# Performance work log

Measured on AMD Instinct MI355X. Metric: run time of the kernel, lower is better.

Reference implementation:

```python
import jax, jax.numpy as jnp
import numpy as np

V, E, U, T, B = 32000, 256, 512, 32, 64

def setup_inputs() -> dict:
    key = jax.random.key(0)
    ks = jax.random.split(key, 12)
    return {
        "input_seq": jax.random.randint(ks[0], (B, T), 1, V),
        "target": jax.random.randint(ks[1], (B, T), 1, V),
        "encoder_output": jax.random.normal(ks[2], (B, T, U), jnp.float32),
        "enc_h": jax.random.normal(ks[3], (B, U), jnp.float32),
        "enc_c": jax.random.normal(ks[4], (B, U), jnp.float32),
        "emb": jax.random.normal(ks[5], (V, E), jnp.float32) * 0.02,
        "Wk": jax.random.normal(ks[6], (E, 4 * U), jnp.float32) * 0.05,
        "Wr": jax.random.normal(ks[7], (U, 4 * U), jnp.float32) * 0.05,
        "b": jnp.zeros((4 * U,), jnp.float32),
        "Wgen": jax.random.normal(ks[8], (2 * U + E, U), jnp.float32) * 0.05,
        "bgen": jnp.zeros((U,), jnp.float32),
    }


def _lstm(x, h0, c0, Wk, Wr, b):
    # x: [B,T,E]; Keras gate order i,f,c,o; returns seq of h [B,T,U], hT, cT
    xg = jnp.einsum('bte,eg->btg', x, Wk) + b  # precompute input projections
    def cell(carry, xg_t):
        h, c = carry
        g = xg_t + h @ Wr
        i, f, cc, o = jnp.split(g, 4, axis=-1)
        c_new = jax.nn.sigmoid(f) * c + jax.nn.sigmoid(i) * jnp.tanh(cc)
        h_new = jax.nn.sigmoid(o) * jnp.tanh(c_new)
        return (h_new, c_new), h_new
    (hT, cT), hs = jax.lax.scan(cell, (h0, c0), jnp.swapaxes(xg, 0, 1))
    return jnp.swapaxes(hs, 0, 1), hT, cT


def reference(input_seq, target, encoder_output, enc_h, enc_c, emb, Wk, Wr, b, Wgen, bgen):
    dec_in0 = emb[target]  # [B,T,E]
    def outer(carry, _):
        dec_in, h, c = carry
        outs, hT, cT = _lstm(dec_in, h, c, Wk, Wr, b)  # [B,T,U]
        h_b = jnp.broadcast_to(h[:, None, :], (B, T, U))  # pre-update state, per original
        feat = jnp.concatenate([encoder_output, h_b, dec_in], axis=-1)
        p_gen = jax.nn.sigmoid(feat @ Wgen + bgen)  # [B,T,U]
        idx = jnp.argmax(outs, axis=-1)  # greedy 'token' ids (as in original)
        new_in = emb[idx]
        return (new_in, hT, cT), (outs, p_gen, h, c)
    _, (dec_outs, p_gens, hs, cs) = jax.lax.scan(
        outer, (dec_in0, enc_h, enc_c), None, length=T - 1)
    return dec_outs, p_gens, hs, cs
```

## Files before the change

### kernel.cpp

```cpp
#include <hip/hip_runtime.h>
#include <math.h>

#define Bz 64
#define Tz 32
#define Uz 512
#define NITER 31
#define G4 2048

typedef unsigned long long ull;

__device__ __forceinline__ float sigf(float x) { return 1.f / (1.f + expf(-x)); }

#define AT_LOADF(p)   __hip_atomic_load((p), __ATOMIC_RELAXED, __HIP_MEMORY_SCOPE_AGENT)
#define AT_LOADI(p)   __hip_atomic_load((p), __ATOMIC_RELAXED, __HIP_MEMORY_SCOPE_AGENT)
#define AT_LOAD64(p)  __hip_atomic_load((p), __ATOMIC_RELAXED, __HIP_MEMORY_SCOPE_AGENT)
#define AT_STORE(p,v) __hip_atomic_store((p), (v), __ATOMIC_RELAXED, __HIP_MEMORY_SCOPE_AGENT)

__device__ __forceinline__ void poll32(const unsigned* fl, unsigned target) {
  const unsigned* f = &fl[(threadIdx.x & 31) * 16];
  unsigned v;
  do {
    v = __hip_atomic_load(f, __ATOMIC_RELAXED, __HIP_MEMORY_SCOPE_AGENT);
  } while (__any((int)(v < target)));
}

__global__ __launch_bounds__(256) void gemm_f32(
    const float* __restrict__ A, const int* __restrict__ Arows, int lda,
    const float* __restrict__ Bm, int ldb, const float* __restrict__ bias,
    float* __restrict__ C, int N, int K)
{
  __shared__ __align__(16) float As[16][68];
  __shared__ __align__(16) float Bs[16][68];
  const int tid = threadIdx.x;
  const int bm = blockIdx.y, bn = blockIdx.x;
  const int tx = tid & 15, ty = tid >> 4;
  float acc[4][4] = {{0.f}};
  const int sm = tid >> 2, sk = (tid & 3) * 4;
  const int arow = Arows ? Arows[bm * 64 + sm] : (bm * 64 + sm);
  const float* Ap = A + (size_t)arow * lda + sk;
  const int bk = tid >> 4, bn4 = (tid & 15) * 4;
  const float* Bp = Bm + (size_t)bk * ldb + bn * 64 + bn4;
  for (int kk = 0; kk < K; kk += 16) {
    float4 av = *(const float4*)(Ap + kk);
    float4 bv = *(const float4*)(Bp + (size_t)kk * ldb);
    As[sk + 0][sm] = av.x; As[sk + 1][sm] = av.y;
    As[sk + 2][sm] = av.z; As[sk + 3][sm] = av.w;
    *(float4*)&Bs[bk][bn4] = bv;
    __syncthreads();
#pragma unroll
    for (int kt = 0; kt < 16; ++kt) {
      float4 a = *(const float4*)&As[kt][ty * 4];
      float4 b = *(const float4*)&Bs[kt][tx * 4];
      acc[0][0] += a.x * b.x; acc[0][1] += a.x * b.y; acc[0][2] += a.x * b.z; acc[0][3] += a.x * b.w;
      acc[1][0] += a.y * b.x; acc[1][1] += a.y * b.y; acc[1][2] += a.y * b.z; acc[1][3] += a.y * b.w;
      acc[2][0] += a.z * b.x; acc[2][1] += a.z * b.y; acc[2][2] += a.z * b.z; acc[2][3] += a.z * b.w;
      acc[3][0] += a.w * b.x; acc[3][1] += a.w * b.y; acc[3][2] += a.w * b.z; acc[3][3] += a.w * b.w;
    }
    __syncthreads();
  }
  const int cm = bm * 64 + ty * 4, cn = bn * 64 + tx * 4;
  float bc0 = bias ? bias[cn + 0] : 0.f;
  float bc1 = bias ? bias[cn + 1] : 0.f;
  float bc2 = bias ? bias[cn + 2] : 0.f;
  float bc3 = bias ? bias[cn + 3] : 0.f;
#pragma unroll
  for (int i = 0; i < 4; ++i) {
    float4 o;
    o.x = acc[i][0] + bc0; o.y = acc[i][1] + bc1;
    o.z = acc[i][2] + bc2; o.w = acc[i][3] + bc3;
    *(float4*)&C[(size_t)(cm + i) * N + cn] = o;
  }
}

__global__ void init_kernel(unsigned* __restrict__ flags) {
  int i = blockIdx.x * blockDim.x + threadIdx.x;
  if (i < 8192) flags[i] = 0u;
}

#define DO_GEMM(HRED, GIDX, GV)                                                          \
  {                                                                                      \
    float4 a0 = {0,0,0,0}, a1 = {0,0,0,0}, a2 = {0,0,0,0}, a3 = {0,0,0,0};               \
    _Pragma("unroll")                                                                    \
    for (int kk = 0; kk < 16; ++kk) {                                                    \
      float4 hv = *(const float4*)&HRED[(kk * 32 + ks) * 4];                             \
      a0.x += hv.x * w4[kk].x; a0.y += hv.x * w4[kk].y;                                  \
      a0.z += hv.x * w4[kk].z; a0.w += hv.x * w4[kk].w;                                  \
      a1.x += hv.y * w4[kk].x; a1.y += hv.y * w4[kk].y;                                  \
      a1.z += hv.y * w4[kk].z; a1.w += hv.y * w4[kk].w;                                  \
      a2.x += hv.z * w4[kk].x; a2.y += hv.z * w4[kk].y;                                  \
      a2.z += hv.z * w4[kk].z; a2.w += hv.z * w4[kk].w;                                  \
      a3.x += hv.w * w4[kk].x; a3.y += hv.w * w4[kk].y;                                  \
      a3.z += hv.w * w4[kk].z; a3.w += hv.w * w4[kk].w;                                  \
    }                                                                                    \
    bool c1 = ks & 1, c2 = ks & 2, c3 = ks & 4, c4 = ks & 8;                             \
    float4 k0 = c1 ? a2 : a0, k1 = c1 ? a3 : a1;                                         \
    float4 s0 = c1 ? a0 : a2, s1 = c1 ? a1 : a3;                                         \
    k0.x += __shfl_xor(s0.x, 2); k0.y += __shfl_xor(s0.y, 2);                            \
    k0.z += __shfl_xor(s0.z, 2); k0.w += __shfl_xor(s0.w, 2);                            \
    k1.x += __shfl_xor(s1.x, 2); k1.y += __shfl_xor(s1.y, 2);                            \
    k1.z += __shfl_xor(s1.z, 2); k1.w += __shfl_xor(s1.w, 2);                            \
    float4 m0 = c2 ? k1 : k0, n0 = c2 ? k0 : k1;                                         \
    m0.x += __shfl_xor(n0.x, 4); m0.y += __shfl_xor(n0.y, 4);                            \
    m0.z += __shfl_xor(n0.z, 4); m0.w += __shfl_xor(n0.w, 4);                            \
    float q0 = c3 ? m0.z : m0.x, q1 = c3 ? m0.w : m0.y;                                  \
    float r0 = c3 ? m0.x : m0.z, r1 = c3 ? m0.y : m0.w;                                  \
    q0 += __shfl_xor(r0, 8); q1 += __shfl_xor(r1, 8);                                    \
    float u_ = c4 ? q1 : q0, v_ = c4 ? q0 : q1;                                          \
    u_ += __shfl_xor(v_, 16);                                                            \
    u_ += __shfl_xor(u_, 32);                                                            \
    if (lane < 32) g_l[GIDX][b_f][j_f] = u_ + (GV);                                      \
  }

__global__ __launch_bounds__(512, 1) void decoder_persist(
    const float* __restrict__ Wr,
    const float* __restrict__ Wgen,
    const float* __restrict__ bgen,
    const float* __restrict__ enc_h,
    const float* __restrict__ enc_c,
    const float* __restrict__ embW,
    const float* __restrict__ xg0,
    const float* __restrict__ enc_part,
    const float* __restrict__ dec0,
    const float* __restrict__ decW,
    float* __restrict__ hbT,
    int*   __restrict__ idxbuf,
    unsigned* __restrict__ flags,
    float* __restrict__ out)
{
  __shared__ __align__(16) float hredA[2048];
  __shared__ __align__(16) float hredB[2048];
  __shared__ __align__(16) float Wgenl[8192];
  __shared__ float g_l[2][4][68];
  __shared__ float hW_l[128];
  __shared__ float redl[512];
  __shared__ int   idx_l[8][32];
  __shared__ float bgen_l[16];

  const int tid = threadIdx.x;
  const int bid = blockIdx.x;
  const int pr = bid >> 5, ug = bid & 31;
  const int bA0 = pr * 4, bB0 = 32 + pr * 4;
  const int u0 = ug * 16;
  const int w = tid >> 6, lane = tid & 63;
  const int ks = lane >> 1, jsub = lane & 1;
  const int jloc = w * 8 + jsub * 4;
  const int gcol0 = (jloc >> 4) * Uz + u0 + (jloc & 15);
  const int b_f = 2 * (ks & 1) + ((ks >> 1) & 1);
  const int ji_f = 2 * ((ks >> 2) & 1) + ((ks >> 3) & 1);
  const int j_f = jloc + ji_f;
  const int gcol_f = (j_f >> 4) * Uz + u0 + (j_f & 15);
  const int p_b = lane >> 4, p_ul = lane & 15;

  float* out_dec = out;
  float* out_pg  = out + (size_t)NITER * Bz * Tz * Uz;
  float* out_hs  = out + 2 * (size_t)NITER * Bz * Tz * Uz;
  float* out_cs  = out_hs + (size_t)NITER * Bz * Uz;

  unsigned* flA = flags + (pr * 2 + 0) * 512;
  unsigned* flB = flags + (pr * 2 + 1) * 512;
  float* hbTp = hbT + pr * 8192;

  float4 w4[16];
#pragma unroll
  for (int kk = 0; kk < 16; ++kk)
    w4[kk] = *(const float4*)&Wr[(size_t)(kk * 32 + ks) * G4 + gcol0];
  for (int q = 0; q < 16; ++q) {
    int e = q * 512 + tid, k = e >> 4, ul = e & 15;
    Wgenl[k * 16 + ul] = Wgen[(size_t)(512 + k) * Uz + u0 + ul];
  }
  if (tid < 16) bgen_l[tid] = bgen[u0 + tid];
  {
    int k = tid;
#pragma unroll
    for (int b = 0; b < 4; ++b) {
      hredA[k * 4 + b] = enc_h[(size_t)(bA0 + b) * Uz + k];
      hredB[k * 4 + b] = enc_h[(size_t)(bB0 + b) * Uz + k];
    }
  }
  float c_reg = 0.f;
  if (w == 0) c_reg = enc_c[(size_t)(bA0 + p_b) * Uz + u0 + p_ul];
  if (w == 1) c_reg = enc_c[(size_t)(bB0 + p_b) * Uz + u0 + p_ul];
  __syncthreads();

#pragma unroll 1
  for (int s = 0; s < NITER; ++s) {
    const int* idxp = idxbuf + ((s + 1) & 1) * 2048;
    int*       idxq = idxbuf + (s & 1) * 2048;
    const unsigned base = 33u * s;

    if (s > 0) {
      if (w == 1 && lane < 32) poll32(flA, base);
      __syncthreads();
      if (tid < 128) {
        int pb = tid >> 4, t2 = (tid & 15) * 2;
        int batch = (pb < 4) ? bA0 + pb : bB0 + (pb - 4);
        idx_l[pb][t2]     = AT_LOADI(&idxp[batch * Tz + t2]);
        idx_l[pb][t2 + 1] = AT_LOADI(&idxp[batch * Tz + t2 + 1]);
      } else if (w >= 2 && w < 6) {
        int st = tid - 128;
        const ull* src = (const ull*)&hbTp[1 * 2048];
        ull* dst = (ull*)hredB;
#pragma unroll
        for (int q = 0; q < 4; ++q) dst[q * 256 + st] = AT_LOAD64(&src[q * 256 + st]);
      }
      __syncthreads();
    }
    {
      int g = tid >> 8, r6 = tid & 255, kq = r6 >> 6, l6 = r6 & 63;
      int b = l6 >> 4, ul = l6 & 15;
      const float* hr = g ? hredB : hredA;
      float a = 0.f;
#pragma unroll 8
      for (int k = kq * 128; k < kq * 128 + 128; ++k)
        a += hr[k * 4 + b] * Wgenl[k * 16 + ul];
      redl[tid] = a;
    }
    __syncthreads();
    if (tid < 128) {
      int g = tid >> 6, l6 = tid & 63;
      hW_l[tid] = (redl[g * 256 + l6] + redl[g * 256 + 64 + l6]) +
                  (redl[g * 256 + 128 + l6] + redl[g * 256 + 192 + l6]);
    }
    if (w < 2) {
      int batch = (w == 0 ? bA0 : bB0) + p_b;
      const float* hr = w ? hredB : hredA;
      out_hs[((size_t)s * Bz + batch) * Uz + u0 + p_ul] = hr[(u0 + p_ul) * 4 + p_b];
      out_cs[((size_t)s * Bz + batch) * Uz + u0 + p_ul] = c_reg;
    }
    __syncthreads();
#pragma unroll 1
    for (int i = 0; i < 8; ++i) {
      int o = i * 512 + tid;
      int ul = o & 15, t = (o >> 4) & 31, pb = o >> 9;
      int batch = (pb < 4) ? bA0 + pb : bB0 + (pb - 4);
      size_t r = (size_t)batch * Tz + t;
      float dv = (s == 0) ? dec0[r * Uz + u0 + ul]
                          : decW[(size_t)idx_l[pb][t] * Uz + u0 + ul];
      float v = enc_part[r * Uz + u0 + ul] + hW_l[(pb >> 2) * 64 + (pb & 3) * 16 + ul]
              + dv + bgen_l[ul];
      out_pg[(((size_t)s * Bz + batch) * Tz + t) * Uz + u0 + ul] = sigf(v);
    }

#pragma unroll 1
    for (int t = 0; t < Tz; ++t) {
      const int gt = s * Tz + t;
      ull stg[16];
      float gvA = 0.f, gvB = 0.f;
      if (lane < 32) {
        int rA = (bA0 + b_f) * Tz + t, rB = (bB0 + b_f) * Tz + t;
        if (s == 0) {
          gvA = xg0[(size_t)rA * G4 + gcol_f];
          gvB = xg0[(size_t)rB * G4 + gcol_f];
        } else {
          gvA = embW[(size_t)idx_l[b_f][t] * G4 + gcol_f];
          gvB = embW[(size_t)idx_l[4 + b_f][t] * G4 + gcol_f];
        }
      }
      if (w == 1 && gt > 0) {
        if (lane < 32) poll32(flB, base + t);
        const ull* src = (const ull*)&hbTp[((gt & 1) * 2 + 1) * 2048];
#pragma unroll
        for (int q = 0; q < 16; ++q) stg[q] = AT_LOAD64(&src[q * 64 + lane]);
      }
      DO_GEMM(hredA, 0, gvA);
      __syncthreads();
      if (w == 0) {
        float gi = g_l[0][p_b][p_ul],      gf = g_l[0][p_b][16 + p_ul];
        float gc = g_l[0][p_b][32 + p_ul], go = g_l[0][p_b][48 + p_ul];
        c_reg = sigf(gf) * c_reg + sigf(gi) * tanhf(gc);
        float hn = sigf(go) * tanhf(c_reg);
        int parw = (gt + 1) & 1;
        AT_STORE(&hbTp[(parw * 2 + 0) * 2048 + (u0 + p_ul) * 4 + p_b], hn);
        AT_STORE(&out_dec[(((size_t)s * Bz + bA0 + p_b) * Tz + t) * Uz + u0 + p_ul], hn);
        asm volatile("s_waitcnt vmcnt(0)" ::: "memory");
        if (lane == 0) AT_STORE(&flA[ug * 16], base + t + 1);
      } else if (w == 1 && gt > 0) {
        ull* dst = (ull*)hredB;
#pragma unroll
        for (int q = 0; q < 16; ++q) dst[q * 64 + lane] = stg[q];
      }
      __syncthreads();
      if (w == 6) {
        if (lane < 32) poll32(flA, base + t + 1);
        const ull* src = (const ull*)&hbTp[(((gt + 1) & 1) * 2 + 0) * 2048];
#pragma unroll
        for (int q = 0; q < 16; ++q) stg[q] = AT_LOAD64(&src[q * 64 + lane]);
      }
      DO_GEMM(hredB, 1, gvB);
      __syncthreads();
      if (w == 1) {
        float gi = g_l[1][p_b][p_ul],      gf = g_l[1][p_b][16 + p_ul];
        float gc = g_l[1][p_b][32 + p_ul], go = g_l[1][p_b][48 + p_ul];
        c_reg = sigf(gf) * c_reg + sigf(gi) * tanhf(gc);
        float hn = sigf(go) * tanhf(c_reg);
        int parw = (gt + 1) & 1;
        AT_STORE(&hbTp[(parw * 2 + 1) * 2048 + (u0 + p_ul) * 4 + p_b], hn);
        AT_STORE(&out_dec[(((size_t)s * Bz + bB0 + p_b) * Tz + t) * Uz + u0 + p_ul], hn);
        asm volatile("s_waitcnt vmcnt(0)" ::: "memory");
        if (lane == 0) AT_STORE(&flB[ug * 16], base + t + 1);
      } else if (w == 6) {
        ull* dst = (ull*)hredA;
#pragma unroll
        for (int q = 0; q < 16; ++q) dst[q * 64 + lane] = stg[q];
      }
      __syncthreads();
    }

    if (s < NITER - 1) {
      if (w == 1 && lane < 32) poll32(flB, base + 32);
      __syncthreads();
      {
        int R = ug * 8 + w;
        int pb = R >> 5, t = R & 31;
        int batch = (pb < 4) ? bA0 + pb : bB0 + (pb - 4);
        const float* row = &out_dec[(((size_t)s * Bz + batch) * Tz + t) * Uz];
        float bv = -3.4e38f; int bi = 0;
#pragma unroll
        for (int q = 0; q < 8; ++q) {
          int u = lane + q * 64;
          float v = AT_LOADF(&row[u]);
          if (v > bv) { bv = v; bi = u; }
        }
#pragma unroll
        for (int off = 1; off < 64; off <<= 1) {
          float ov = __shfl_xor(bv, off);
          int   oi = __shfl_xor(bi, off);
          if (ov > bv || (ov == bv && oi < bi)) { bv = ov; bi = oi; }
        }
        if (lane == 0) AT_STORE(&idxq[batch * Tz + t], bi);
      }
      asm volatile("s_waitcnt vmcnt(0)" ::: "memory");
      __syncthreads();
      if (tid == 0) {
        AT_STORE(&flA[ug * 16], base + 33);
        AT_STORE(&flB[ug * 16], base + 33);
      }
    }
  }
}

extern "C" void kernel_launch(void* const* d_in, const int* in_sizes, int n_in,
                              void* d_out, int out_size, void* d_ws, size_t ws_size,
                              hipStream_t stream) {
  const int*   target = (const int*)d_in[1];
  const float* enc    = (const float*)d_in[2];
  const float* enc_h  = (const float*)d_in[3];
  const float* enc_cp = (const float*)d_in[4];
  const float* emb    = (const float*)d_in[5];
  const float* Wk     = (const float*)d_in[6];
  const float* Wr     = (const float*)d_in[7];
  const float* bb     = (const float*)d_in[8];
  const float* Wgen   = (const float*)d_in[9];
  const float* bgen   = (const float*)d_in[10];
  float* out = (float*)d_out;

  float* ws = (float*)d_ws;
  float* hbT      = ws;
  float* embW     = ws + 65536;
  float* xg0      = ws + 1114112;
  float* enc_part = ws + 5308416;
  float* dec0     = ws + 6356992;
  float* decW     = ws + 7405568;
  int*   idxbuf   = (int*)(ws + 7667712);
  unsigned* flags = (unsigned*)(ws + 7671808);

  init_kernel<<<16, 512, 0, stream>>>(flags);
  gemm_f32<<<dim3(32, 8), 256, 0, stream>>>(emb, nullptr, 256, Wk, 2048, bb, embW, 2048, 256);
  gemm_f32<<<dim3(32, 32), 256, 0, stream>>>(emb, target, 256, Wk, 2048, bb, xg0, 2048, 256);
  gemm_f32<<<dim3(8, 32), 256, 0, stream>>>(enc, nullptr, 512, Wgen, 512, nullptr, enc_part, 512, 512);
  gemm_f32<<<dim3(8, 32), 256, 0, stream>>>(emb, target, 256, Wgen + 1024 * 512, 512, nullptr, dec0, 512, 256);
  gemm_f32<<<dim3(8, 8), 256, 0, stream>>>(emb, nullptr, 256, Wgen + 1024 * 512, 512, nullptr, decW, 512, 256);

  decoder_persist<<<256, 512, 0, stream>>>(Wr, Wgen, bgen, enc_h, enc_cp, embW, xg0,
      enc_part, dec0, decW, hbT, idxbuf, flags, out);
}
```

Measured before the change: 5.819 ms.

## Replace flag polling with sequence-tagged mailboxes and compute argmax locally per block

Hidden-state exchange between blocks now packs each h value with its global step tag into a 64-bit mailbox word. Consumers spin directly on the data, with loads issued before the GEMM and retried after it, so the separate flag store, vmcnt wait and flag poll are gone. The per-outer-iteration global argmax phase and its extra barrier are replaced by each block computing argmax from its replicated LDS copy of h as the steps go. This also removes the flag-init kernel. The risks are reliance on the tag values never colliding with stale workspace contents across launches, and heavier spin traffic from four waves polling.

```diff
diff --git a/kernel.cpp b/kernel.cpp
--- a/kernel.cpp
+++ b/kernel.cpp
@@ -11,18 +11,8 @@
 
 __device__ __forceinline__ float sigf(float x) { return 1.f / (1.f + expf(-x)); }
 
-#define AT_LOADF(p)   __hip_atomic_load((p), __ATOMIC_RELAXED, __HIP_MEMORY_SCOPE_AGENT)
-#define AT_LOADI(p)   __hip_atomic_load((p), __ATOMIC_RELAXED, __HIP_MEMORY_SCOPE_AGENT)
-#define AT_LOAD64(p)  __hip_atomic_load((p), __ATOMIC_RELAXED, __HIP_MEMORY_SCOPE_AGENT)
-#define AT_STORE(p,v) __hip_atomic_store((p), (v), __ATOMIC_RELAXED, __HIP_MEMORY_SCOPE_AGENT)
-
-__device__ __forceinline__ void poll32(const unsigned* fl, unsigned target) {
-  const unsigned* f = &fl[(threadIdx.x & 31) * 16];
-  unsigned v;
-  do {
-    v = __hip_atomic_load(f, __ATOMIC_RELAXED, __HIP_MEMORY_SCOPE_AGENT);
-  } while (__any((int)(v < target)));
-}
+#define AT_LOAD64(p)    __hip_atomic_load((p), __ATOMIC_RELAXED, __HIP_MEMORY_SCOPE_AGENT)
+#define AT_STORE64(p,v) __hip_atomic_store((p), (v), __ATOMIC_RELAXED, __HIP_MEMORY_SCOPE_AGENT)
 
 __global__ __launch_bounds__(256) void gemm_f32(
     const float* __restrict__ A, const int* __restrict__ Arows, int lda,
@@ -70,11 +60,6 @@
     o.z = acc[i][2] + bc2; o.w = acc[i][3] + bc3;
     *(float4*)&C[(size_t)(cm + i) * N + cn] = o;
   }
-}
-
-__global__ void init_kernel(unsigned* __restrict__ flags) {
-  int i = blockIdx.x * blockDim.x + threadIdx.x;
-  if (i < 8192) flags[i] = 0u;
 }
 
 #define DO_GEMM(HRED, GIDX, GV)                                                          \
@@ -111,6 +96,53 @@
     if (lane < 32) g_l[GIDX][b_f][j_f] = u_ + (GV);                                      \
   }
 
+#define MAIL_ISSUE(SV, SRC)                                                              \
+  _Pragma("unroll")                                                                      \
+  for (int q = 0; q < 8; ++q) SV[q] = AT_LOAD64(&(SRC)[sidx8 + q]);
+
+#define MAIL_RETRY(SV, SRC, TG)                                                          \
+  for (;;) {                                                                             \
+    int bad = 0;                                                                         \
+    _Pragma("unroll")                                                                    \
+    for (int q = 0; q < 8; ++q) bad |= ((unsigned)(SV[q] >> 32) != (TG));                \
+    if (!__any(bad)) break;                                                              \
+    _Pragma("unroll")                                                                    \
+    for (int q = 0; q < 8; ++q)                                                          \
+      if ((unsigned)(SV[q] >> 32) != (TG)) SV[q] = AT_LOAD64(&(SRC)[sidx8 + q]);         \
+  }
+
+#define MAIL2LDS(SV, DST)                                                                \
+  {                                                                                      \
+    float4 f0, f1;                                                                       \
+    f0.x = __uint_as_float((unsigned)SV[0]); f0.y = __uint_as_float((unsigned)SV[1]);    \
+    f0.z = __uint_as_float((unsigned)SV[2]); f0.w = __uint_as_float((unsigned)SV[3]);    \
+    f1.x = __uint_as_float((unsigned)SV[4]); f1.y = __uint_as_float((unsigned)SV[5]);    \
+    f1.z = __uint_as_float((unsigned)SV[6]); f1.w = __uint_as_float((unsigned)SV[7]);    \
+    *(float4*)&(DST)[sidx8] = f0; *(float4*)&(DST)[sidx8 + 4] = f1;                      \
+  }
+
+#define ARGMAX2(HRED, PBOFF, TT, SP)                                                     \
+  {                                                                                      \
+    _Pragma("unroll")                                                                    \
+    for (int half = 0; half < 2; ++half) {                                               \
+      int b = (w - 6) * 2 + half;                                                        \
+      float bv = -3.4e38f; int bi = 0;                                                   \
+      _Pragma("unroll")                                                                  \
+      for (int q = 0; q < 8; ++q) {                                                      \
+        int u = lane + q * 64;                                                           \
+        float v = (HRED)[u * 4 + b];                                                     \
+        if (v > bv) { bv = v; bi = u; }                                                  \
+      }                                                                                  \
+      _Pragma("unroll")                                                                  \
+      for (int off = 1; off < 64; off <<= 1) {                                           \
+        float ov = __shfl_xor(bv, off);                                                  \
+        int   oi = __shfl_xor(bi, off);                                                  \
+        if (ov > bv || (ov == bv && oi < bi)) { bv = ov; bi = oi; }                      \
+      }                                                                                  \
+      if (lane == 0) idx_l[SP][(PBOFF) + b][TT] = bi;                                    \
+    }                                                                                    \
+  }
+
 __global__ __launch_bounds__(512, 1) void decoder_persist(
     const float* __restrict__ Wr,
     const float* __restrict__ Wgen,
@@ -122,9 +154,7 @@
     const float* __restrict__ enc_part,
     const float* __restrict__ dec0,
     const float* __restrict__ decW,
-    float* __restrict__ hbT,
-    int*   __restrict__ idxbuf,
-    unsigned* __restrict__ flags,
+    ull*   __restrict__ mail,
     float* __restrict__ out)
 {
   __shared__ __align__(16) float hredA[2048];
@@ -133,7 +163,7 @@
   __shared__ float g_l[2][4][68];
   __shared__ float hW_l[128];
   __shared__ float redl[512];
-  __shared__ int   idx_l[8][32];
+  __shared__ int   idx_l[2][8][32];
   __shared__ float bgen_l[16];
 
   const int tid = threadIdx.x;
@@ -150,15 +180,15 @@
   const int j_f = jloc + ji_f;
   const int gcol_f = (j_f >> 4) * Uz + u0 + (j_f & 15);
   const int p_b = lane >> 4, p_ul = lane & 15;
+  const int sidx8 = ((w - 2) * 64 + lane) * 8;
 
   float* out_dec = out;
   float* out_pg  = out + (size_t)NITER * Bz * Tz * Uz;
   float* out_hs  = out + 2 * (size_t)NITER * Bz * Tz * Uz;
   float* out_cs  = out_hs + (size_t)NITER * Bz * Uz;
 
-  unsigned* flA = flags + (pr * 2 + 0) * 512;
-  unsigned* flB = flags + (pr * 2 + 1) * 512;
-  float* hbTp = hbT + pr * 8192;
+  ull* mA[2] = { mail + (size_t)(0 * 8 + pr) * 2048, mail + (size_t)(1 * 8 + pr) * 2048 };
+  ull* mB[2] = { mail + (size_t)(2 * 8 + pr) * 2048, mail + (size_t)(3 * 8 + pr) * 2048 };
 
   float4 w4[16];
 #pragma unroll
@@ -184,27 +214,31 @@
 
 #pragma unroll 1
   for (int s = 0; s < NITER; ++s) {
-    const int* idxp = idxbuf + ((s + 1) & 1) * 2048;
-    int*       idxq = idxbuf + (s & 1) * 2048;
-    const unsigned base = 33u * s;
-
-    if (s > 0) {
-      if (w == 1 && lane < 32) poll32(flA, base);
-      __syncthreads();
-      if (tid < 128) {
-        int pb = tid >> 4, t2 = (tid & 15) * 2;
-        int batch = (pb < 4) ? bA0 + pb : bB0 + (pb - 4);
-        idx_l[pb][t2]     = AT_LOADI(&idxp[batch * Tz + t2]);
-        idx_l[pb][t2 + 1] = AT_LOADI(&idxp[batch * Tz + t2 + 1]);
-      } else if (w >= 2 && w < 6) {
-        int st = tid - 128;
-        const ull* src = (const ull*)&hbTp[1 * 2048];
-        ull* dst = (ull*)hredB;
-#pragma unroll
-        for (int q = 0; q < 4; ++q) dst[q * 256 + st] = AT_LOAD64(&src[q * 256 + st]);
-      }
-      __syncthreads();
-    }
+    const int sp = s & 1;
+    const int rp = sp ^ 1;
+    ull sv[8];
+
+    if (s > 0 && w >= 2 && w < 6) {
+      const ull* src = mB[0];
+      MAIL_ISSUE(sv, src);
+      MAIL_RETRY(sv, src, (unsigned)(32 * s));
+    }
+    if (w == 0) {
+      int batch = bA0 + p_b;
+      out_hs[((size_t)s * Bz + batch) * Uz + u0 + p_ul] = hredA[(u0 + p_ul) * 4 + p_b];
+      out_cs[((size_t)s * Bz + batch) * Uz + u0 + p_ul] = c_reg;
+    }
+    if (s > 0 && (w == 6 || w == 7)) ARGMAX2(hredA, 0, 31, rp);
+    __syncthreads();
+    if (s > 0 && w >= 2 && w < 6) MAIL2LDS(sv, hredB);
+    __syncthreads();
+    if (w == 1) {
+      int batch = bB0 + p_b;
+      out_hs[((size_t)s * Bz + batch) * Uz + u0 + p_ul] = hredB[(u0 + p_ul) * 4 + p_b];
+      out_cs[((size_t)s * Bz + batch) * Uz + u0 + p_ul] = c_reg;
+    }
+    if (s > 0 && (w == 6 || w == 7)) ARGMAX2(hredB, 4, 31, rp);
+    __syncthreads();
     {
       int g = tid >> 8, r6 = tid & 255, kq = r6 >> 6, l6 = r6 & 63;
       int b = l6 >> 4, ul = l6 & 15;
@@ -221,12 +255,6 @@
       hW_l[tid] = (redl[g * 256 + l6] + redl[g * 256 + 64 + l6]) +
                   (redl[g * 256 + 128 + l6] + redl[g * 256 + 192 + l6]);
     }
-    if (w < 2) {
-      int batch = (w == 0 ? bA0 : bB0) + p_b;
-      const float* hr = w ? hredB : hredA;
-      out_hs[((size_t)s * Bz + batch) * Uz + u0 + p_ul] = hr[(u0 + p_ul) * 4 + p_b];
-      out_cs[((size_t)s * Bz + batch) * Uz + u0 + p_ul] = c_reg;
-    }
     __syncthreads();
 #pragma unroll 1
     for (int i = 0; i < 8; ++i) {
@@ -235,16 +263,17 @@
       int batch = (pb < 4) ? bA0 + pb : bB0 + (pb - 4);
       size_t r = (size_t)batch * Tz + t;
       float dv = (s == 0) ? dec0[r * Uz + u0 + ul]
-                          : decW[(size_t)idx_l[pb][t] * Uz + u0 + ul];
+                          : decW[(size_t)idx_l[rp][pb][t] * Uz + u0 + ul];
       float v = enc_part[r * Uz + u0 + ul] + hW_l[(pb >> 2) * 64 + (pb & 3) * 16 + ul]
               + dv + bgen_l[ul];
       out_pg[(((size_t)s * Bz + batch) * Tz + t) * Uz + u0 + ul] = sigf(v);
     }
+    __syncthreads();
 
 #pragma unroll 1
     for (int t = 0; t < Tz; ++t) {
       const int gt = s * Tz + t;
-      ull stg[16];
+      const unsigned tgo = (unsigned)(gt + 1);
       float gvA = 0.f, gvB = 0.f;
       if (lane < 32) {
         int rA = (bA0 + b_f) * Tz + t, rB = (bB0 + b_f) * Tz + t;
@@ -252,89 +281,56 @@
           gvA = xg0[(size_t)rA * G4 + gcol_f];
           gvB = xg0[(size_t)rB * G4 + gcol_f];
         } else {
-          gvA = embW[(size_t)idx_l[b_f][t] * G4 + gcol_f];
-          gvB = embW[(size_t)idx_l[4 + b_f][t] * G4 + gcol_f];
+          gvA = embW[(size_t)idx_l[rp][b_f][t] * G4 + gcol_f];
+          gvB = embW[(size_t)idx_l[rp][4 + b_f][t] * G4 + gcol_f];
         }
       }
-      if (w == 1 && gt > 0) {
-        if (lane < 32) poll32(flB, base + t);
-        const ull* src = (const ull*)&hbTp[((gt & 1) * 2 + 1) * 2048];
-#pragma unroll
-        for (int q = 0; q < 16; ++q) stg[q] = AT_LOAD64(&src[q * 64 + lane]);
-      }
-      DO_GEMM(hredA, 0, gvA);
+      if (t > 0 && w >= 2 && w < 6) {
+        const ull* src = mB[gt & 1];
+        MAIL_ISSUE(sv, src);
+        DO_GEMM(hredA, 0, gvA);
+        MAIL_RETRY(sv, src, (unsigned)gt);
+      } else {
+        DO_GEMM(hredA, 0, gvA);
+      }
       __syncthreads();
       if (w == 0) {
         float gi = g_l[0][p_b][p_ul],      gf = g_l[0][p_b][16 + p_ul];
         float gc = g_l[0][p_b][32 + p_ul], go = g_l[0][p_b][48 + p_ul];
         c_reg = sigf(gf) * c_reg + sigf(gi) * tanhf(gc);
         float hn = sigf(go) * tanhf(c_reg);
-        int parw = (gt + 1) & 1;
-        AT_STORE(&hbTp[(parw * 2 + 0) * 2048 + (u0 + p_ul) * 4 + p_b], hn);
-        AT_STORE(&out_dec[(((size_t)s * Bz + bA0 + p_b) * Tz + t) * Uz + u0 + p_ul], hn);
-        asm volatile("s_waitcnt vmcnt(0)" ::: "memory");
-        if (lane == 0) AT_STORE(&flA[ug * 16], base + t + 1);
-      } else if (w == 1 && gt > 0) {
-        ull* dst = (ull*)hredB;
-#pragma unroll
-        for (int q = 0; q < 16; ++q) dst[q * 64 + lane] = stg[q];
+        AT_STORE64(&mA[tgo & 1][(u0 + p_ul) * 4 + p_b],
+                   ((ull)tgo << 32) | (ull)__float_as_uint(hn));
+        out_dec[(((size_t)s * Bz + bA0 + p_b) * Tz + t) * Uz + u0 + p_ul] = hn;
+      } else if (t > 0 && w >= 2 && w < 6) {
+        MAIL2LDS(sv, hredB);
+      } else if (t > 0 && (w == 6 || w == 7)) {
+        ARGMAX2(hredA, 0, t - 1, sp);
       }
       __syncthreads();
-      if (w == 6) {
-        if (lane < 32) poll32(flA, base + t + 1);
-        const ull* src = (const ull*)&hbTp[(((gt + 1) & 1) * 2 + 0) * 2048];
-#pragma unroll
-        for (int q = 0; q < 16; ++q) stg[q] = AT_LOAD64(&src[q * 64 + lane]);
-      }
-      DO_GEMM(hredB, 1, gvB);
+      if (w >= 2 && w < 6) {
+        const ull* src = mA[tgo & 1];
+        MAIL_ISSUE(sv, src);
+        DO_GEMM(hredB, 1, gvB);
+        MAIL_RETRY(sv, src, tgo);
+      } else {
+        DO_GEMM(hredB, 1, gvB);
+      }
       __syncthreads();
       if (w == 1) {
         float gi = g_l[1][p_b][p_ul],      gf = g_l[1][p_b][16 + p_ul];
         float gc = g_l[1][p_b][32 + p_ul], go = g_l[1][p_b][48 + p_ul];
         c_reg = sigf(gf) * c_reg + sigf(gi) * tanhf(gc);
         float hn = sigf(go) * tanhf(c_reg);
-        int parw = (gt + 1) & 1;
-        AT_STORE(&hbTp[(parw * 2 + 1) * 2048 + (u0 + p_ul) * 4 + p_b], hn);
-        AT_STORE(&out_dec[(((size_t)s * Bz + bB0 + p_b) * Tz + t) * Uz + u0 + p_ul], hn);
-        asm volatile("s_waitcnt vmcnt(0)" ::: "memory");
-        if (lane == 0) AT_STORE(&flB[ug * 16], base + t + 1);
-      } else if (w == 6) {
-        ull* dst = (ull*)hredA;
-#pragma unroll
-        for (int q = 0; q < 16; ++q) dst[q * 64 + lane] = stg[q];
+        AT_STORE64(&mB[tgo & 1][(u0 + p_ul) * 4 + p_b],
+                   ((ull)tgo << 32) | (ull)__float_as_uint(hn));
+        out_dec[(((size_t)s * Bz + bB0 + p_b) * Tz + t) * Uz + u0 + p_ul] = hn;
+      } else if (w >= 2 && w < 6) {
+        MAIL2LDS(sv, hredA);
+      } else if (t > 0 && (w == 6 || w == 7)) {
+        ARGMAX2(hredB, 4, t - 1, sp);
       }
       __syncthreads();
-    }
-
-    if (s < NITER - 1) {
-      if (w == 1 && lane < 32) poll32(flB, base + 32);
-      __syncthreads();
-      {
-        int R = ug * 8 + w;
-        int pb = R >> 5, t = R & 31;
-        int batch = (pb < 4) ? bA0 + pb : bB0 + (pb - 4);
-        const float* row = &out_dec[(((size_t)s * Bz + batch) * Tz + t) * Uz];
-        float bv = -3.4e38f; int bi = 0;
-#pragma unroll
-        for (int q = 0; q < 8; ++q) {
-          int u = lane + q * 64;
-          float v = AT_LOADF(&row[u]);
-          if (v > bv) { bv = v; bi = u; }
-        }
-#pragma unroll
-        for (int off = 1; off < 64; off <<= 1) {
-          float ov = __shfl_xor(bv, off);
-          int   oi = __shfl_xor(bi, off);
-          if (ov > bv || (ov == bv && oi < bi)) { bv = ov; bi = oi; }
-        }
-        if (lane == 0) AT_STORE(&idxq[batch * Tz + t], bi);
-      }
-      asm volatile("s_waitcnt vmcnt(0)" ::: "memory");
-      __syncthreads();
-      if (tid == 0) {
-        AT_STORE(&flA[ug * 16], base + 33);
-        AT_STORE(&flB[ug * 16], base + 33);
-      }
     }
   }
 }
@@ -355,16 +351,13 @@
   float* out = (float*)d_out;
 
   float* ws = (float*)d_ws;
-  float* hbT      = ws;
-  float* embW     = ws + 65536;
-  float* xg0      = ws + 1114112;
-  float* enc_part = ws + 5308416;
-  float* dec0     = ws + 6356992;
-  float* decW     = ws + 7405568;
-  int*   idxbuf   = (int*)(ws + 7667712);
-  unsigned* flags = (unsigned*)(ws + 7671808);
-
-  init_kernel<<<16, 512, 0, stream>>>(flags);
+  ull*   mail     = (ull*)ws;
+  float* embW     = ws + 131072;
+  float* xg0      = ws + 1179648;
+  float* enc_part = ws + 5373952;
+  float* dec0     = ws + 6422528;
+  float* decW     = ws + 7471104;
+
   gemm_f32<<<dim3(32, 8), 256, 0, stream>>>(emb, nullptr, 256, Wk, 2048, bb, embW, 2048, 256);
   gemm_f32<<<dim3(32, 32), 256, 0, stream>>>(emb, target, 256, Wk, 2048, bb, xg0, 2048, 256);
   gemm_f32<<<dim3(8, 32), 256, 0, stream>>>(enc, nullptr, 512, Wgen, 512, nullptr, enc_part, 512, 512);
@@ -372,5 +365,5 @@
   gemm_f32<<<dim3(8, 8), 256, 0, stream>>>(emb, nullptr, 256, Wgen + 1024 * 512, 512, nullptr, decW, 512, 256);
 
   decoder_persist<<<256, 512, 0, stream>>>(Wr, Wgen, bgen, enc_h, enc_cp, embW, xg0,
-      enc_part, dec0, decW, hbT, idxbuf, flags, out);
+      enc_part, dec0, decW, mail, out);
 }
```

Measured after the change: 6.500 ms. 1.12x slower.
